# Performance work log

Hardware: AMD Instinct MI355X
Metric: run time of the kernel (lower is better)

The kernel has to match this reference:

```python
import jax, jax.numpy as jnp
import numpy as np

B, L, D, H = 2, 2048, 1024, 16
DK = D // H


def setup_inputs() -> dict:
    key = jax.random.key(0)
    ks = jax.random.split(key, 12)
    s = 1.0 / np.sqrt(D)
    inp = {
        "query": jax.random.normal(ks[0], (B, L, D), jnp.float32),
        "key_": jax.random.normal(ks[1], (B, L, D), jnp.float32),
        "value": jax.random.normal(ks[2], (B, L, D), jnp.float32),
        # causal boolean mask, broadcast over heads: (B, 1, L_q, L_k)
        "mask": jnp.broadcast_to(jnp.tril(jnp.ones((L, L), jnp.bool_)), (B, 1, L, L)),
        "w_q": jax.random.uniform(ks[3], (D, D), jnp.float32, -s, s),
        "b_q": jax.random.uniform(ks[4], (D,), jnp.float32, -s, s),
        "w_k": jax.random.uniform(ks[5], (D, D), jnp.float32, -s, s),
        "b_k": jax.random.uniform(ks[6], (D,), jnp.float32, -s, s),
        "w_v": jax.random.uniform(ks[7], (D, D), jnp.float32, -s, s),
        "b_v": jax.random.uniform(ks[8], (D,), jnp.float32, -s, s),
        "w_o": jax.random.uniform(ks[9], (D, D), jnp.float32, -s, s),
        "b_o": jax.random.uniform(ks[10], (D,), jnp.float32, -s, s),
    }
    return inp


def reference(query, key_, value, mask, w_q, b_q, w_k, b_k, w_v, b_v, w_o, b_o):
    # torch nn.Linear: y = x @ W.T + b, weight shape (out, in)
    Q = query @ w_q.T + b_q
    K = key_ @ w_k.T + b_k
    V = value @ w_v.T + b_v
    # (B, L, H, DK) -> (B, H, L, DK)
    Q = Q.reshape(B, L, H, DK).transpose(0, 2, 1, 3)
    K = K.reshape(B, L, H, DK).transpose(0, 2, 1, 3)
    V = V.reshape(B, L, H, DK).transpose(0, 2, 1, 3)
    scaling = jnp.sqrt(jnp.float32(DK))
    scores = jnp.einsum("bhqd,bhkd->bhqk", Q, K) / scaling  # (B,H,L,L)
    scores = jnp.where(mask, scores, jnp.float32(-1e9))
    attn = jax.nn.softmax(scores, axis=-1)
    out = jnp.einsum("bhqk,bhkd->bhqd", attn, V)  # (B,H,L,DK)
    out = out.transpose(0, 2, 1, 3).reshape(B, L, D)
    return out @ w_o.T + b_o
```

## Files before the change

### kernel.cpp

```cpp
#include <hip/hip_runtime.h>
#include <stdint.h>

#define Bb 2
#define Ll 2048
#define Dd 1024
#define Hh 16
#define DKd 64
#define Mm (Bb*Ll)

typedef __bf16 bf16_t;
typedef __bf16 bf16x8 __attribute__((ext_vector_type(8)));
typedef float f32x4 __attribute__((ext_vector_type(4)));
typedef unsigned u32x2 __attribute__((ext_vector_type(2)));

#define AS1C(p) ((const __attribute__((address_space(1))) void*)(p))
#define AS3(p)  ((__attribute__((address_space(3))) void*)(p))

__device__ __forceinline__ unsigned short bfu(float f){
  return __builtin_bit_cast(unsigned short, (bf16_t)f);
}

struct CvtArgs { const float* in[4]; ushort4* out[4]; };

__global__ void cvt_multi(CvtArgs a, int n4){
  const int z = blockIdx.y;
  const float* in = a.in[z];
  ushort4* out = a.out[z];
  int i = blockIdx.x*256 + threadIdx.x;
  if (i < n4){
    float4 v = ((const float4*)in)[i];
    ushort4 o; o.x=bfu(v.x); o.y=bfu(v.y); o.z=bfu(v.z); o.w=bfu(v.w);
    out[i] = o;
  }
}

__global__ __launch_bounds__(256) void transpose_v(const bf16_t* __restrict__ Vh,
                                                   bf16_t* __restrict__ VT){
  __shared__ bf16_t Tl[64][72];
  const int bh = blockIdx.y;
  const int l0 = blockIdx.x * 64;
  const int tid = threadIdx.x;
  const bf16_t* src = Vh + (size_t)bh*Ll*DKd;
  bf16_t* dst = VT + (size_t)bh*Ll*DKd;
#pragma unroll
  for (int rd = 0; rd < 2; ++rd){
    int l = rd*32 + (tid>>3), dk0 = (tid&7)*8;
    bf16x8 v = *(const bf16x8*)(src + (size_t)(l0+l)*DKd + dk0);
#pragma unroll
    for (int j = 0; j < 8; ++j) Tl[dk0+j][l] = v[j];
  }
  __syncthreads();
#pragma unroll
  for (int rd = 0; rd < 2; ++rd){
    int dk = rd*32 + (tid>>3), lc = (tid&7)*8;
    *(bf16x8*)(dst + (size_t)dk*Ll + l0 + lc) = *(const bf16x8*)&Tl[dk][lc];
  }
}

#define BM 128
#define BN 64
#define BKs 64

struct GemmArgs {
  const bf16_t* A[3];
  const bf16_t* W[3];
  const float*  bias[3];
  void*         out[3];
  float         scale[3];
};

__device__ __forceinline__ void stage_tile(
    const bf16_t* __restrict__ A, const bf16_t* __restrict__ Bw,
    int m0, int n0, int K, int k0, bf16_t* As, bf16_t* Bs,
    int w, int srow, int scol)
{
#pragma unroll
  for (int i = 0; i < 4; i++) {
    int c = i*4 + w;
    int row = c*8 + srow;
    int sc = scol ^ ((row & 7) << 3);
    __builtin_amdgcn_global_load_lds(AS1C(A + (size_t)(m0+row)*K + k0 + sc),
                                     AS3(As + c*512), 16, 0, 0);
  }
#pragma unroll
  for (int i = 0; i < 2; i++) {
    int c = i*4 + w;
    int row = c*8 + srow;
    int sc = scol ^ ((row & 7) << 3);
    __builtin_amdgcn_global_load_lds(AS1C(Bw + (size_t)(n0+row)*K + k0 + sc),
                                     AS3(Bs + c*512), 16, 0, 0);
  }
}

template<int OUTMODE>
__global__ __launch_bounds__(256) void gemm_bt(GemmArgs ga, int M, int N, int K)
{
  const int z = blockIdx.z;
  const bf16_t* __restrict__ A  = ga.A[z];
  const bf16_t* __restrict__ Bw = ga.W[z];
  const float*  __restrict__ bias = ga.bias[z];
  void* __restrict__ out = ga.out[z];
  const float scale = ga.scale[z];

  __shared__ bf16_t As[2][BM*BKs];
  __shared__ bf16_t Bs[2][BN*BKs];
  const int tid = threadIdx.x;
  const int lane = tid & 63;
  const int w = tid >> 6;
  const int m0 = blockIdx.x * BM;
  const int n0 = blockIdx.y * BN;
  const int wr = (w >> 1) * 64, wc = (w & 1) * 32;
  const int lrow16 = lane & 15;
  const int kgrp = lane >> 4;
  const int srow = lane >> 3;
  const int scol = (lane & 7) * 8;

  f32x4 acc[4][2] = {};

  stage_tile(A, Bw, m0, n0, K, 0, As[0], Bs[0], w, srow, scol);
  __syncthreads();

  int cur = 0;
  for (int k0 = 0; k0 < K; k0 += BKs) {
    if (k0 + BKs < K)
      stage_tile(A, Bw, m0, n0, K, k0 + BKs, As[cur^1], Bs[cur^1], w, srow, scol);
#pragma unroll
    for (int ks = 0; ks < 2; ++ks) {
      const int kbyte = ks*64 + kgrp*16;
      bf16x8 af[4], bfr[2];
#pragma unroll
      for (int m = 0; m < 4; m++) {
        int row = wr + m*16 + lrow16;
        af[m] = *(const bf16x8*)((const char*)As[cur] + row*128 + (kbyte ^ ((row & 7) << 4)));
      }
#pragma unroll
      for (int n = 0; n < 2; n++) {
        int row = wc + n*16 + lrow16;
        bfr[n] = *(const bf16x8*)((const char*)Bs[cur] + row*128 + (kbyte ^ ((row & 7) << 4)));
      }
#pragma unroll
      for (int m = 0; m < 4; m++)
#pragma unroll
        for (int n = 0; n < 2; n++)
          acc[m][n] = __builtin_amdgcn_mfma_f32_16x16x32_bf16(af[m], bfr[n], acc[m][n], 0, 0, 0);
    }
    __syncthreads();
    cur ^= 1;
  }

#pragma unroll
  for (int m = 0; m < 4; m++)
#pragma unroll
    for (int n = 0; n < 2; n++)
#pragma unroll
      for (int i = 0; i < 4; i++) {
        int row = m0 + wr + m*16 + kgrp*4 + i;
        int col = n0 + wc + n*16 + lrow16;
        float v = (acc[m][n][i] + bias[col]) * scale;
        if (OUTMODE == 1) {
          ((float*)out)[(size_t)row*N + col] = v;
        } else {
          int b = row >> 11, l = row & 2047;
          int h = col >> 6, dk = col & 63;
          ((unsigned short*)out)[((size_t)((b<<4) + h)*Ll + l)*DKd + dk] = bfu(v);
        }
      }
}

#define KVB 64

__global__ __launch_bounds__(256) void attn_kernel(
    const bf16_t* __restrict__ Qh, const bf16_t* __restrict__ Kh,
    const bf16_t* __restrict__ VTg, unsigned short* __restrict__ Oa)
{
  const int id = blockIdx.x;
  const int x = id & 7;
  const int mm = id >> 3;
  const int j = mm & 31, hq = mm >> 5;
  int qt;
  switch (hq) {
    case 0:  qt = j;            break;
    case 1:  qt = 31 - j;       break;
    case 2:  qt = (j + 16) & 31; break;
    default: qt = (15 - j) & 31; break;
  }
  const int bh = x + 8*hq;
  const int q0 = qt * 64;

  const int tid = threadIdx.x, lane = tid & 63, w = tid >> 6;
  const int r = lane & 15, g = lane >> 4;

  const bf16_t* Qp  = Qh  + (size_t)bh * Ll * DKd;
  const bf16_t* Kp  = Kh  + (size_t)bh * Ll * DKd;
  const bf16_t* VTp = VTg + (size_t)bh * Ll * DKd;

  __shared__ bf16_t Klds[2][64*64];
  __shared__ bf16_t Vlds[2][64*64];
  __shared__ bf16_t Plds[4][16*64];

  const int qbase = q0 + w*16;
  bf16x8 qf[2];
#pragma unroll
  for (int ks = 0; ks < 2; ++ks)
    qf[ks] = *(const bf16x8*)(Qp + (size_t)(qbase + r)*DKd + ks*32 + g*8);

  bf16x8 ones;
#pragma unroll
  for (int jj = 0; jj < 8; ++jj) ones[jj] = (bf16_t)1.0f;

  f32x4 accO[4] = {};
  f32x4 accL = {};
  float mrow = -1e30f;

  const int krow_l = lane >> 3;
  const int kcol_l = ((lane & 7)*16) ^ (krow_l << 4);
  char* Pw = (char*)&Plds[w][0];
  const int rsw = (r & 7) << 4;

  const int nkv = qt + 1;

#pragma unroll
  for (int i = 0; i < 2; ++i) {
    int c = i*4 + w;
    __builtin_amdgcn_global_load_lds(
      AS1C((const char*)Kp + (size_t)(c*8 + krow_l)*128 + kcol_l),
      AS3((char*)&Klds[0][0] + c*1024), 16, 0, 0);
    __builtin_amdgcn_global_load_lds(
      AS1C((const char*)VTp + (size_t)(c*8 + krow_l)*4096 + kcol_l),
      AS3((char*)&Vlds[0][0] + c*1024), 16, 0, 0);
  }
  __syncthreads();

  int cur = 0;
  for (int t = 0; t < nkv; ++t) {
    const int kv0 = t * KVB;
    if (t + 1 < nkv) {
#pragma unroll
      for (int i = 0; i < 2; ++i) {
        int c = i*4 + w;
        __builtin_amdgcn_global_load_lds(
          AS1C((const char*)Kp + (size_t)(kv0 + KVB + c*8 + krow_l)*128 + kcol_l),
          AS3((char*)&Klds[cur^1][0] + c*1024), 16, 0, 0);
        __builtin_amdgcn_global_load_lds(
          AS1C((const char*)VTp + (size_t)(c*8 + krow_l)*4096 + (kv0 + KVB)*2 + kcol_l),
          AS3((char*)&Vlds[cur^1][0] + c*1024), 16, 0, 0);
      }
    }

    const char* Kbase = (const char*)&Klds[cur][0];
    f32x4 s[4] = {};
    __builtin_amdgcn_s_setprio(1);
#pragma unroll
    for (int ks = 0; ks < 2; ++ks) {
      const int kbyte = ks*64 + g*16;
#pragma unroll
      for (int n = 0; n < 4; ++n) {
        int row = n*16 + r;
        bf16x8 kf = *(const bf16x8*)(Kbase + row*128 + (kbyte ^ ((row & 7) << 4)));
        s[n] = __builtin_amdgcn_mfma_f32_16x16x32_bf16(kf, qf[ks], s[n], 0, 0, 0);
      }
    }
    __builtin_amdgcn_s_setprio(0);

    if (t == nkv - 1) {
      const int qg = qbase + r;
#pragma unroll
      for (int n = 0; n < 4; ++n)
#pragma unroll
        for (int i = 0; i < 4; ++i)
          if (kv0 + n*16 + g*4 + i > qg) s[n][i] = -1e30f;
    }

    float mx = fmaxf(fmaxf(fmaxf(s[0][0], s[0][1]), s[0][2]),
                     fmaxf(fmaxf(s[0][3], s[1][0]), s[1][1]));
    mx = fmaxf(mx, fmaxf(fmaxf(s[1][2], s[1][3]), fmaxf(s[2][0], s[2][1])));
    mx = fmaxf(mx, fmaxf(fmaxf(s[2][2], s[2][3]), fmaxf(s[3][0], s[3][1])));
    mx = fmaxf(mx, fmaxf(s[3][2], s[3][3]));
    if (__any(mx > mrow + 8.f)) {
      mx = fmaxf(mx, __shfl_xor(mx, 16));
      mx = fmaxf(mx, __shfl_xor(mx, 32));
      float mnew = fmaxf(mrow, mx);
      float corr = exp2f(mrow - mnew);
      float c0 = __shfl(corr, g*4 + 0);
      float c1 = __shfl(corr, g*4 + 1);
      float c2 = __shfl(corr, g*4 + 2);
      float c3 = __shfl(corr, g*4 + 3);
#pragma unroll
      for (int n = 0; n < 4; ++n) {
        accO[n][0] *= c0; accO[n][1] *= c1; accO[n][2] *= c2; accO[n][3] *= c3;
      }
      accL[0] *= c0; accL[1] *= c1; accL[2] *= c2; accL[3] *= c3;
      mrow = mnew;
    }
#pragma unroll
    for (int n = 0; n < 4; ++n)
#pragma unroll
      for (int i = 0; i < 4; ++i)
        s[n][i] = exp2f(s[n][i] - mrow);

#pragma unroll
    for (int n = 0; n < 4; ++n) {
      unsigned lo = (unsigned)bfu(s[n][0]) | ((unsigned)bfu(s[n][1]) << 16);
      unsigned hi = (unsigned)bfu(s[n][2]) | ((unsigned)bfu(s[n][3]) << 16);
      u32x2 pk; pk[0] = lo; pk[1] = hi;
      *(u32x2*)(Pw + r*128 + ((n*32 + g*8) ^ rsw)) = pk;
    }

    const char* Vbase = (const char*)&Vlds[cur][0];
    __builtin_amdgcn_s_setprio(1);
#pragma unroll
    for (int ks = 0; ks < 2; ++ks) {
      const int kbyte = ks*64 + g*16;
      bf16x8 pa = *(const bf16x8*)(Pw + r*128 + (kbyte ^ rsw));
      accL = __builtin_amdgcn_mfma_f32_16x16x32_bf16(pa, ones, accL, 0, 0, 0);
#pragma unroll
      for (int n = 0; n < 4; ++n) {
        int row = n*16 + r;
        bf16x8 vf = *(const bf16x8*)(Vbase + row*128 + (kbyte ^ ((row & 7) << 4)));
        accO[n] = __builtin_amdgcn_mfma_f32_16x16x32_bf16(pa, vf, accO[n], 0, 0, 0);
      }
    }
    __builtin_amdgcn_s_setprio(0);
    __syncthreads();
    cur ^= 1;
  }

  const int b = bh >> 4, h = bh & 15;
#pragma unroll
  for (int i = 0; i < 4; ++i) {
    float inv = 1.f / accL[i];
    int q = qbase + g*4 + i;
#pragma unroll
    for (int n = 0; n < 4; ++n)
      Oa[((size_t)(b*Ll + q))*Dd + h*DKd + n*16 + r] = bfu(accO[n][i] * inv);
  }
}

extern "C" void kernel_launch(void* const* d_in, const int* in_sizes, int n_in,
                              void* d_out, int out_size, void* d_ws, size_t ws_size,
                              hipStream_t stream)
{
  const float* q  = (const float*)d_in[0];
  const float* k  = (const float*)d_in[1];
  const float* v  = (const float*)d_in[2];
  const float* wq = (const float*)d_in[4];
  const float* bq = (const float*)d_in[5];
  const float* wk = (const float*)d_in[6];
  const float* bk = (const float*)d_in[7];
  const float* wv = (const float*)d_in[8];
  const float* bv = (const float*)d_in[9];
  const float* wo = (const float*)d_in[10];
  const float* bo = (const float*)d_in[11];

  char* ws = (char*)d_ws;
  bf16_t* Xq = (bf16_t*)(ws + 0);
  bf16_t* Xk = (bf16_t*)(ws + 8388608);
  bf16_t* Xv = (bf16_t*)(ws + 16777216);
  bf16_t* Wq = (bf16_t*)(ws + 25165824);
  bf16_t* Wk = (bf16_t*)(ws + 27262976);
  bf16_t* Wv = (bf16_t*)(ws + 29360128);
  bf16_t* Wo = (bf16_t*)(ws + 31457280);
  bf16_t* Qh = (bf16_t*)(ws + 33554432);
  bf16_t* Kh = (bf16_t*)(ws + 41943040);
  bf16_t* Vh = (bf16_t*)(ws + 50331648);
  bf16_t* Oa = (bf16_t*)(ws + 58720256);
  bf16_t* VT = Xq;

  const int NX = Mm * Dd;
  const int NW = Dd * Dd;

  CvtArgs cx; cx.in[0]=q; cx.in[1]=k; cx.in[2]=v; cx.in[3]=q;
  cx.out[0]=(ushort4*)Xq; cx.out[1]=(ushort4*)Xk; cx.out[2]=(ushort4*)Xv; cx.out[3]=(ushort4*)Xq;
  cvt_multi<<<dim3(NX/4/256, 3), 256, 0, stream>>>(cx, NX/4);

  CvtArgs cw; cw.in[0]=wq; cw.in[1]=wk; cw.in[2]=wv; cw.in[3]=wo;
  cw.out[0]=(ushort4*)Wq; cw.out[1]=(ushort4*)Wk; cw.out[2]=(ushort4*)Wv; cw.out[3]=(ushort4*)Wo;
  cvt_multi<<<dim3(NW/4/256, 4), 256, 0, stream>>>(cw, NW/4);

  const float qscale = 0.125f * 1.4426950408889634f;
  GemmArgs gqkv;
  gqkv.A[0]=Xq; gqkv.A[1]=Xk; gqkv.A[2]=Xv;
  gqkv.W[0]=Wq; gqkv.W[1]=Wk; gqkv.W[2]=Wv;
  gqkv.bias[0]=bq; gqkv.bias[1]=bk; gqkv.bias[2]=bv;
  gqkv.out[0]=Qh; gqkv.out[1]=Kh; gqkv.out[2]=Vh;
  gqkv.scale[0]=qscale; gqkv.scale[1]=1.0f; gqkv.scale[2]=1.0f;
  gemm_bt<0><<<dim3(Mm/BM, Dd/BN, 3), 256, 0, stream>>>(gqkv, Mm, Dd, Dd);

  transpose_v<<<dim3(32, 32), 256, 0, stream>>>(Vh, VT);

  attn_kernel<<<dim3(1024), 256, 0, stream>>>(Qh, Kh, VT, (unsigned short*)Oa);

  GemmArgs go;
  go.A[0]=Oa; go.A[1]=Oa; go.A[2]=Oa;
  go.W[0]=Wo; go.W[1]=Wo; go.W[2]=Wo;
  go.bias[0]=bo; go.bias[1]=bo; go.bias[2]=bo;
  go.out[0]=d_out; go.out[1]=d_out; go.out[2]=d_out;
  go.scale[0]=1.0f; go.scale[1]=1.0f; go.scale[2]=1.0f;
  gemm_bt<1><<<dim3(Mm/BM, Dd/BN, 1), 256, 0, stream>>>(go, Mm, Dd, Dd);
}
```

Baseline: 133.8 us.

## Pair causal query tiles per attention block and use explicit vmcnt waits

Each attention block now handles two query tiles, j and 31-j, back to back, so every block runs exactly 33 KV iterations and the causal triangle is balanced across 512 blocks instead of 1024 uneven ones. The K/V prefetch keeps streaming across the tile switch, and the first tile's output is written mid-loop before the accumulators are reset. The GEMM and attention loops replace __syncthreads with explicit s_waitcnt vmcnt plus raw barriers so the next tile's loads stay in flight. exp2f becomes the hardware exp2 intrinsic. Halving the grid may lower occupancy or tail parallelism, and the hand-counted vmcnt values must match the number of outstanding loads.

```diff
diff --git a/kernel.cpp b/kernel.cpp
--- a/kernel.cpp
+++ b/kernel.cpp
@@ -18,6 +18,14 @@
 
 __device__ __forceinline__ unsigned short bfu(float f){
   return __builtin_bit_cast(unsigned short, (bf16_t)f);
+}
+__device__ __forceinline__ void wait_vm4(){ asm volatile("s_waitcnt vmcnt(4)" ::: "memory"); }
+__device__ __forceinline__ void wait_vm6(){ asm volatile("s_waitcnt vmcnt(6)" ::: "memory"); }
+__device__ __forceinline__ void wait_vm0(){ asm volatile("s_waitcnt vmcnt(0)" ::: "memory"); }
+__device__ __forceinline__ void bar(){
+  __builtin_amdgcn_sched_barrier(0);
+  __builtin_amdgcn_s_barrier();
+  __builtin_amdgcn_sched_barrier(0);
 }
 
 struct CvtArgs { const float* in[4]; ushort4* out[4]; };
@@ -118,12 +126,17 @@
   f32x4 acc[4][2] = {};
 
   stage_tile(A, Bw, m0, n0, K, 0, As[0], Bs[0], w, srow, scol);
-  __syncthreads();
-
+
+  const int KT = K / BKs;
   int cur = 0;
-  for (int k0 = 0; k0 < K; k0 += BKs) {
-    if (k0 + BKs < K)
-      stage_tile(A, Bw, m0, n0, K, k0 + BKs, As[cur^1], Bs[cur^1], w, srow, scol);
+  for (int kt = 0; kt < KT; ++kt) {
+    if (kt + 1 < KT) {
+      stage_tile(A, Bw, m0, n0, K, (kt+1)*BKs, As[cur^1], Bs[cur^1], w, srow, scol);
+      wait_vm6();
+    } else {
+      wait_vm0();
+    }
+    bar();
 #pragma unroll
     for (int ks = 0; ks < 2; ++ks) {
       const int kbyte = ks*64 + kgrp*16;
@@ -144,7 +157,7 @@
         for (int n = 0; n < 2; n++)
           acc[m][n] = __builtin_amdgcn_mfma_f32_16x16x32_bf16(af[m], bfr[n], acc[m][n], 0, 0, 0);
     }
-    __syncthreads();
+    bar();
     cur ^= 1;
   }
 
@@ -175,17 +188,11 @@
 {
   const int id = blockIdx.x;
   const int x = id & 7;
-  const int mm = id >> 3;
-  const int j = mm & 31, hq = mm >> 5;
-  int qt;
-  switch (hq) {
-    case 0:  qt = j;            break;
-    case 1:  qt = 31 - j;       break;
-    case 2:  qt = (j + 16) & 31; break;
-    default: qt = (15 - j) & 31; break;
-  }
+  const int rest = id >> 3;
+  const int hq = rest >> 4;
+  const int j  = rest & 15;
   const int bh = x + 8*hq;
-  const int q0 = qt * 64;
+  const int qtA = j, qtB = 31 - j;
 
   const int tid = threadIdx.x, lane = tid & 63, w = tid >> 6;
   const int r = lane & 15, g = lane >> 4;
@@ -198,11 +205,13 @@
   __shared__ bf16_t Vlds[2][64*64];
   __shared__ bf16_t Plds[4][16*64];
 
-  const int qbase = q0 + w*16;
-  bf16x8 qf[2];
-#pragma unroll
-  for (int ks = 0; ks < 2; ++ks)
-    qf[ks] = *(const bf16x8*)(Qp + (size_t)(qbase + r)*DKd + ks*32 + g*8);
+  bf16x8 qf[2], qB[2];
+#pragma unroll
+  for (int ks = 0; ks < 2; ++ks) {
+    qf[ks] = *(const bf16x8*)(Qp + (size_t)(qtA*64 + w*16 + r)*DKd + ks*32 + g*8);
+    qB[ks] = *(const bf16x8*)(Qp + (size_t)(qtB*64 + w*16 + r)*DKd + ks*32 + g*8);
+  }
+  int qb = qtA*64 + w*16;
 
   bf16x8 ones;
 #pragma unroll
@@ -216,39 +225,38 @@
   const int kcol_l = ((lane & 7)*16) ^ (krow_l << 4);
   char* Pw = (char*)&Plds[w][0];
   const int rsw = (r & 7) << 4;
-
-  const int nkv = qt + 1;
-
-#pragma unroll
-  for (int i = 0; i < 2; ++i) {
-    int c = i*4 + w;
-    __builtin_amdgcn_global_load_lds(
-      AS1C((const char*)Kp + (size_t)(c*8 + krow_l)*128 + kcol_l),
-      AS3((char*)&Klds[0][0] + c*1024), 16, 0, 0);
-    __builtin_amdgcn_global_load_lds(
-      AS1C((const char*)VTp + (size_t)(c*8 + krow_l)*4096 + kcol_l),
-      AS3((char*)&Vlds[0][0] + c*1024), 16, 0, 0);
-  }
-  __syncthreads();
+  const int b_ = bh >> 4, h_ = bh & 15;
+
+  auto pre_tiles = [&](int kv, int buf){
+#pragma unroll
+    for (int i = 0; i < 2; ++i) {
+      int c = i*4 + w;
+      __builtin_amdgcn_global_load_lds(
+        AS1C((const char*)Kp + (size_t)(kv*KVB + c*8 + krow_l)*128 + kcol_l),
+        AS3((char*)&Klds[buf][0] + c*1024), 16, 0, 0);
+      __builtin_amdgcn_global_load_lds(
+        AS1C((const char*)VTp + (size_t)(c*8 + krow_l)*4096 + kv*128 + kcol_l),
+        AS3((char*)&Vlds[buf][0] + c*1024), 16, 0, 0);
+    }
+  };
+
+  pre_tiles(0, 0);
 
   int cur = 0;
-  for (int t = 0; t < nkv; ++t) {
-    const int kv0 = t * KVB;
-    if (t + 1 < nkv) {
-#pragma unroll
-      for (int i = 0; i < 2; ++i) {
-        int c = i*4 + w;
-        __builtin_amdgcn_global_load_lds(
-          AS1C((const char*)Kp + (size_t)(kv0 + KVB + c*8 + krow_l)*128 + kcol_l),
-          AS3((char*)&Klds[cur^1][0] + c*1024), 16, 0, 0);
-        __builtin_amdgcn_global_load_lds(
-          AS1C((const char*)VTp + (size_t)(c*8 + krow_l)*4096 + (kv0 + KVB)*2 + kcol_l),
-          AS3((char*)&Vlds[cur^1][0] + c*1024), 16, 0, 0);
-      }
-    }
+  for (int s = 0; s < 33; ++s) {
+    if (s < 32) {
+      int kv2 = (s < j) ? s + 1 : s - j;
+      pre_tiles(kv2, cur^1);
+      wait_vm4();
+    } else {
+      wait_vm0();
+    }
+    bar();
+
+    const int kv0 = ((s <= j) ? s : s - j - 1) * KVB;
 
     const char* Kbase = (const char*)&Klds[cur][0];
-    f32x4 s[4] = {};
+    f32x4 sv[4] = {};
     __builtin_amdgcn_s_setprio(1);
 #pragma unroll
     for (int ks = 0; ks < 2; ++ks) {
@@ -257,30 +265,31 @@
       for (int n = 0; n < 4; ++n) {
         int row = n*16 + r;
         bf16x8 kf = *(const bf16x8*)(Kbase + row*128 + (kbyte ^ ((row & 7) << 4)));
-        s[n] = __builtin_amdgcn_mfma_f32_16x16x32_bf16(kf, qf[ks], s[n], 0, 0, 0);
+        sv[n] = __builtin_amdgcn_mfma_f32_16x16x32_bf16(kf, qf[ks], sv[n], 0, 0, 0);
       }
     }
     __builtin_amdgcn_s_setprio(0);
 
-    if (t == nkv - 1) {
-      const int qg = qbase + r;
+    if (s == j || s == 32) {
+      const int qg = qb + r;
 #pragma unroll
       for (int n = 0; n < 4; ++n)
 #pragma unroll
         for (int i = 0; i < 4; ++i)
-          if (kv0 + n*16 + g*4 + i > qg) s[n][i] = -1e30f;
-    }
-
-    float mx = fmaxf(fmaxf(fmaxf(s[0][0], s[0][1]), s[0][2]),
-                     fmaxf(fmaxf(s[0][3], s[1][0]), s[1][1]));
-    mx = fmaxf(mx, fmaxf(fmaxf(s[1][2], s[1][3]), fmaxf(s[2][0], s[2][1])));
-    mx = fmaxf(mx, fmaxf(fmaxf(s[2][2], s[2][3]), fmaxf(s[3][0], s[3][1])));
-    mx = fmaxf(mx, fmaxf(s[3][2], s[3][3]));
+          if (kv0 + n*16 + g*4 + i > qg) sv[n][i] = -1e30f;
+    }
+
+    float m0 = fmaxf(fmaxf(sv[0][0], sv[0][1]), sv[0][2]);
+    float m1 = fmaxf(fmaxf(sv[0][3], sv[1][0]), sv[1][1]);
+    float m2 = fmaxf(fmaxf(sv[1][2], sv[1][3]), sv[2][0]);
+    float m3 = fmaxf(fmaxf(sv[2][1], sv[2][2]), sv[2][3]);
+    float m4 = fmaxf(fmaxf(sv[3][0], sv[3][1]), sv[3][2]);
+    float mx = fmaxf(fmaxf(fmaxf(m0, m1), m2), fmaxf(fmaxf(m3, m4), sv[3][3]));
     if (__any(mx > mrow + 8.f)) {
       mx = fmaxf(mx, __shfl_xor(mx, 16));
       mx = fmaxf(mx, __shfl_xor(mx, 32));
       float mnew = fmaxf(mrow, mx);
-      float corr = exp2f(mrow - mnew);
+      float corr = __builtin_amdgcn_exp2f(mrow - mnew);
       float c0 = __shfl(corr, g*4 + 0);
       float c1 = __shfl(corr, g*4 + 1);
       float c2 = __shfl(corr, g*4 + 2);
@@ -296,12 +305,12 @@
     for (int n = 0; n < 4; ++n)
 #pragma unroll
       for (int i = 0; i < 4; ++i)
-        s[n][i] = exp2f(s[n][i] - mrow);
+        sv[n][i] = __builtin_amdgcn_exp2f(sv[n][i] - mrow);
 
 #pragma unroll
     for (int n = 0; n < 4; ++n) {
-      unsigned lo = (unsigned)bfu(s[n][0]) | ((unsigned)bfu(s[n][1]) << 16);
-      unsigned hi = (unsigned)bfu(s[n][2]) | ((unsigned)bfu(s[n][3]) << 16);
+      unsigned lo = (unsigned)bfu(sv[n][0]) | ((unsigned)bfu(sv[n][1]) << 16);
+      unsigned hi = (unsigned)bfu(sv[n][2]) | ((unsigned)bfu(sv[n][3]) << 16);
       u32x2 pk; pk[0] = lo; pk[1] = hi;
       *(u32x2*)(Pw + r*128 + ((n*32 + g*8) ^ rsw)) = pk;
     }
@@ -321,18 +330,35 @@
       }
     }
     __builtin_amdgcn_s_setprio(0);
-    __syncthreads();
+
+    if (s == j) {
+#pragma unroll
+      for (int i = 0; i < 4; ++i) {
+        float inv = 1.f / accL[i];
+        int q = qb + g*4 + i;
+#pragma unroll
+        for (int n = 0; n < 4; ++n)
+          Oa[((size_t)(b_*Ll + q))*Dd + h_*DKd + n*16 + r] = bfu(accO[n][i] * inv);
+      }
+#pragma unroll
+      for (int n = 0; n < 4; ++n) accO[n] = f32x4{};
+      accL = f32x4{};
+      mrow = -1e30f;
+      qf[0] = qB[0]; qf[1] = qB[1];
+      qb = qtB*64 + w*16;
+    }
+
+    bar();
     cur ^= 1;
   }
 
-  const int b = bh >> 4, h = bh & 15;
 #pragma unroll
   for (int i = 0; i < 4; ++i) {
     float inv = 1.f / accL[i];
-    int q = qbase + g*4 + i;
+    int q = qb + g*4 + i;
 #pragma unroll
     for (int n = 0; n < 4; ++n)
-      Oa[((size_t)(b*Ll + q))*Dd + h*DKd + n*16 + r] = bfu(accO[n][i] * inv);
+      Oa[((size_t)(b_*Ll + q))*Dd + h_*DKd + n*16 + r] = bfu(accO[n][i] * inv);
   }
 }
 
@@ -388,7 +414,7 @@
 
   transpose_v<<<dim3(32, 32), 256, 0, stream>>>(Vh, VT);
 
-  attn_kernel<<<dim3(1024), 256, 0, stream>>>(Qh, Kh, VT, (unsigned short*)Oa);
+  attn_kernel<<<dim3(512), 256, 0, stream>>>(Qh, Kh, VT, (unsigned short*)Oa);
 
   GemmArgs go;
   go.A[0]=Oa; go.A[1]=Oa; go.A[2]=Oa;
```

Result: faster. 121.9 us (-8.9%).
